# Kernel optimization log

Measured on AMD Instinct MI355X. Metric: run time of the kernel, lower is better.

The kernel has to match this reference:

```python
import jax, jax.numpy as jnp
import numpy as np

V, D, H, L, S_MAX = 32000, 1024, 16, 4, 1024
HD = D // H          # head dim = 64
FF = 4 * D           # mlp hidden = 4096
B, S = 2, 1024


def _layernorm(x, w, b, eps=1e-5):
    mu = jnp.mean(x, axis=-1, keepdims=True)
    var = jnp.mean(jnp.square(x - mu), axis=-1, keepdims=True)
    return (x - mu) * jax.lax.rsqrt(var + eps) * w + b


def setup_inputs() -> dict:
    key = jax.random.key(0)
    ks = jax.random.split(key, 16)
    r = lambda k, shape: (jax.random.normal(k, shape, dtype=jnp.float32) * 0.02)
    return {
        "input_ids": jax.random.randint(ks[0], (B, S), 0, V),
        "tok_emb": r(ks[1], (V, D)),
        "pos_emb": r(ks[2], (S_MAX, D)),
        "ln1_w": jnp.ones((L, D)), "ln1_b": jnp.zeros((L, D)),
        "ln2_w": jnp.ones((L, D)), "ln2_b": jnp.zeros((L, D)),
        "q_w": r(ks[3], (L, D, D)), "q_b": jnp.zeros((L, D)),
        "k_w": r(ks[4], (L, D, D)), "k_b": jnp.zeros((L, D)),
        "v_w": r(ks[5], (L, D, D)), "v_b": jnp.zeros((L, D)),
        "o_w": r(ks[6], (L, D, D)), "o_b": jnp.zeros((L, D)),
        "fc1_w": r(ks[7], (L, FF, D)), "fc1_b": jnp.zeros((L, FF)),
        "fc2_w": r(ks[8], (L, D, FF)), "fc2_b": jnp.zeros((L, D)),
        "lnf_w": jnp.ones((D,)), "lnf_b": jnp.zeros((D,)),
        "head_w": r(ks[9], (V, D)),
    }


def reference(input_ids, tok_emb, pos_emb, ln1_w, ln1_b, ln2_w, ln2_b,
              q_w, q_b, k_w, k_b, v_w, v_b, o_w, o_b,
              fc1_w, fc1_b, fc2_w, fc2_b, lnf_w, lnf_b, head_w):
    b, s = input_ids.shape
    x = tok_emb[input_ids] + pos_emb[:s][None, :, :]          # [B,S,D]
    causal = jnp.tril(jnp.ones((s, s), dtype=bool))           # [S,S]
    scale = 1.0 / np.sqrt(HD)
    for i in range(L):
        # --- causal MHA block ---
        h = _layernorm(x, ln1_w[i], ln1_b[i])
        q = (h @ q_w[i].T + q_b[i]).reshape(b, s, H, HD)
        k = (h @ k_w[i].T + k_b[i]).reshape(b, s, H, HD)
        v = (h @ v_w[i].T + v_b[i]).reshape(b, s, H, HD)
        scores = jnp.einsum('bqhd,bkhd->bhqk', q, k) * scale  # [B,H,S,S]
        scores = jnp.where(causal[None, None], scores, -jnp.inf)
        attn = jax.nn.softmax(scores, axis=-1)
        y = jnp.einsum('bhqk,bkhd->bqhd', attn, v).reshape(b, s, D)
        x = x + (y @ o_w[i].T + o_b[i])
        # --- GELU MLP block (exact gelu, matching torch F.gelu default) ---
        h = _layernorm(x, ln2_w[i], ln2_b[i])
        h = jax.nn.gelu(h @ fc1_w[i].T + fc1_b[i], approximate=False)
        x = x + (h @ fc2_w[i].T + fc2_b[i])
    x = _layernorm(x, lnf_w, lnf_b)
    logits = x[:, -1, :] @ head_w.T                           # [B,V]
    return logits
```

## Files before the change

### kernel.cpp

```cpp
#include <hip/hip_runtime.h>

#define V_SIZE 32000
#define D_DIM  1024
#define H_HEADS 16
#define L_LAYERS 4
#define HD_DIM 64
#define FF_DIM 4096
#define B_BATCH 2
#define S_SEQ  1024
#define M_ROWS (B_BATCH*S_SEQ)
#define KSPL   2

typedef short  s16x8 __attribute__((ext_vector_type(8)));
typedef unsigned short u16x8 __attribute__((ext_vector_type(8)));
typedef float  f32x4 __attribute__((ext_vector_type(4)));
typedef unsigned short u16;
typedef unsigned int   u32;

__device__ inline u16 f2bf(float f){
    u32 u = __float_as_uint(f);
    return (u16)((u + 0x7FFFu + ((u >> 16) & 1u)) >> 16);
}

__device__ inline float gelu_f(float v){
    float y = 0.7978845608f * (v + 0.044715f*v*v*v);
    y = fmaxf(-15.f, fminf(15.f, y));
    float u = __expf(-2.f*y);
    return v / (1.f + u);
}

__device__ inline char* lds_swz(void* base, int row, int byteoff){
    return (char*)base + row*128 + (byteoff ^ ((row & 7) << 4));
}

__device__ inline void gload16(const u16* g, u16* l){
    __builtin_amdgcn_global_load_lds(
        (const __attribute__((address_space(1))) void*)g,
        (__attribute__((address_space(3))) void*)l, 16, 0, 0);
}

__device__ inline int swz_src_col(int lin){
    int row = lin >> 3, s8 = lin & 7;
    return (s8*8) ^ ((row & 7) << 3);
}

__device__ inline s16x8 cvt8(float4 a, float4 b){
    s16x8 o;
    o[0]=(short)f2bf(a.x); o[1]=(short)f2bf(a.y);
    o[2]=(short)f2bf(a.z); o[3]=(short)f2bf(a.w);
    o[4]=(short)f2bf(b.x); o[5]=(short)f2bf(b.y);
    o[6]=(short)f2bf(b.z); o[7]=(short)f2bf(b.w);
    return o;
}

__global__ __launch_bounds__(256) void cvt_flat_k(
    const float* __restrict__ src, u16* __restrict__ dst)
{
    long i = ((long)blockIdx.x*256 + threadIdx.x) * 16;
    float4 v0 = *(const float4*)(src + i);
    float4 v1 = *(const float4*)(src + i + 4);
    float4 v2 = *(const float4*)(src + i + 8);
    float4 v3 = *(const float4*)(src + i + 12);
    *(s16x8*)(dst + i)     = cvt8(v0, v1);
    *(s16x8*)(dst + i + 8) = cvt8(v2, v3);
}

__global__ __launch_bounds__(256) void cvt_qkv_k(
    const float* __restrict__ qw, const float* __restrict__ kw,
    const float* __restrict__ vw, u16* __restrict__ dst)
{
    const long M1 = 1L << 20;
    const int which = blockIdx.y;
    const float* src = (which==0) ? qw : ((which==1) ? kw : vw);
    long i = ((long)blockIdx.x*256 + threadIdx.x) * 16;
    long layer = i >> 20, rem = i & (M1 - 1);
    u16* d = dst + layer*3*M1 + which*M1 + rem;
    float4 v0 = *(const float4*)(src + i);
    float4 v1 = *(const float4*)(src + i + 4);
    float4 v2 = *(const float4*)(src + i + 8);
    float4 v3 = *(const float4*)(src + i + 12);
    *(s16x8*)(d)     = cvt8(v0, v1);
    *(s16x8*)(d + 8) = cvt8(v2, v3);
}

__global__ __launch_bounds__(256) void embed_ln_k(
    const int* __restrict__ ids, const float* __restrict__ tok,
    const float* __restrict__ pos, const float* __restrict__ lw,
    const float* __restrict__ lb, float* __restrict__ x, u16* __restrict__ h)
{
    int row = blockIdx.x;
    int id  = ids[row];
    int s   = row & (S_SEQ - 1);
    int t   = threadIdx.x;
    float4 tv = *(const float4*)(tok + (size_t)id * D_DIM + t*4);
    float4 pv = *(const float4*)(pos + (size_t)s  * D_DIM + t*4);
    float4 vv;
    vv.x = tv.x + pv.x; vv.y = tv.y + pv.y; vv.z = tv.z + pv.z; vv.w = tv.w + pv.w;
    *(float4*)(x + (size_t)row * D_DIM + t*4) = vv;
    float sm  = vv.x + vv.y + vv.z + vv.w;
    float ss = vv.x*vv.x + vv.y*vv.y + vv.z*vv.z + vv.w*vv.w;
#pragma unroll
    for (int off = 1; off < 64; off <<= 1){
        sm += __shfl_xor(sm, off);
        ss += __shfl_xor(ss, off);
    }
    __shared__ float red[8];
    const int wid = t >> 6, lane = t & 63;
    if (lane == 0){ red[wid] = sm; red[4 + wid] = ss; }
    __syncthreads();
    sm = red[0] + red[1] + red[2] + red[3];
    ss = red[4] + red[5] + red[6] + red[7];
    float mu   = sm * (1.0f/1024.0f);
    float rstd = rsqrtf(ss * (1.0f/1024.0f) - mu*mu + 1e-5f);
    float4 wv = *(const float4*)(lw + t*4);
    float4 bv = *(const float4*)(lb + t*4);
    uint2 pk;
    pk.x = (u32)f2bf((vv.x-mu)*rstd*wv.x + bv.x) | ((u32)f2bf((vv.y-mu)*rstd*wv.y + bv.y) << 16);
    pk.y = (u32)f2bf((vv.z-mu)*rstd*wv.z + bv.z) | ((u32)f2bf((vv.w-mu)*rstd*wv.w + bv.w) << 16);
    *(uint2*)(h + (size_t)row * D_DIM + t*4) = pk;
}

__global__ __launch_bounds__(256) void layernorm_f_k(
    const float* __restrict__ x, const float* __restrict__ w, const float* __restrict__ bb,
    float* __restrict__ outF)
{
    const int row = blockIdx.x * S_SEQ + S_SEQ - 1;
    const int t = threadIdx.x;
    float4 vv = *(const float4*)(x + (size_t)row * D_DIM + t*4);
    float s  = vv.x + vv.y + vv.z + vv.w;
    float ss = vv.x*vv.x + vv.y*vv.y + vv.z*vv.z + vv.w*vv.w;
#pragma unroll
    for (int off = 1; off < 64; off <<= 1){
        s  += __shfl_xor(s,  off);
        ss += __shfl_xor(ss, off);
    }
    __shared__ float red[8];
    const int wid = t >> 6, lane = t & 63;
    if (lane == 0){ red[wid] = s; red[4 + wid] = ss; }
    __syncthreads();
    s  = red[0] + red[1] + red[2] + red[3];
    ss = red[4] + red[5] + red[6] + red[7];
    float mu   = s * (1.0f/1024.0f);
    float rstd = rsqrtf(ss * (1.0f/1024.0f) - mu*mu + 1e-5f);
    float4 wv = *(const float4*)(w  + t*4);
    float4 bv = *(const float4*)(bb + t*4);
    float4 o;
    o.x = (vv.x - mu)*rstd*wv.x + bv.x;
    o.y = (vv.y - mu)*rstd*wv.y + bv.y;
    o.z = (vv.z - mu)*rstd*wv.z + bv.z;
    o.w = (vv.w - mu)*rstd*wv.w + bv.w;
    *(float4*)(outF + (size_t)blockIdx.x * D_DIM + t*4) = o;
}

template<int DOLN>
__global__ __launch_bounds__(256) void reduce_ln_k(
    const float* __restrict__ part, const float* __restrict__ bias,
    float* __restrict__ x,
    const float* __restrict__ lw, const float* __restrict__ lb,
    u16* __restrict__ h)
{
    const int row = blockIdx.x, t = threadIdx.x;
    const size_t off = (size_t)row * D_DIM + t*4;
    float4 a = *(float4*)(x + off);
    float4 bv = *(const float4*)(bias + t*4);
    a.x += bv.x; a.y += bv.y; a.z += bv.z; a.w += bv.w;
#pragma unroll
    for (int si = 0; si < KSPL; si++){
        float4 pv = *(const float4*)(part + (size_t)si * M_ROWS * D_DIM + off);
        a.x += pv.x; a.y += pv.y; a.z += pv.z; a.w += pv.w;
    }
    *(float4*)(x + off) = a;
    if (DOLN){
        float sm = a.x + a.y + a.z + a.w;
        float ss = a.x*a.x + a.y*a.y + a.z*a.z + a.w*a.w;
#pragma unroll
        for (int o2 = 1; o2 < 64; o2 <<= 1){
            sm += __shfl_xor(sm, o2);
            ss += __shfl_xor(ss, o2);
        }
        __shared__ float red[8];
        const int wid = t >> 6, lane = t & 63;
        if (lane == 0){ red[wid] = sm; red[4 + wid] = ss; }
        __syncthreads();
        sm = red[0] + red[1] + red[2] + red[3];
        ss = red[4] + red[5] + red[6] + red[7];
        float mu   = sm * (1.0f/1024.0f);
        float rstd = rsqrtf(ss * (1.0f/1024.0f) - mu*mu + 1e-5f);
        float4 wv = *(const float4*)(lw + t*4);
        float4 lbv = *(const float4*)(lb + t*4);
        uint2 pk;
        pk.x = (u32)f2bf((a.x-mu)*rstd*wv.x + lbv.x) | ((u32)f2bf((a.y-mu)*rstd*wv.y + lbv.y) << 16);
        pk.y = (u32)f2bf((a.z-mu)*rstd*wv.z + lbv.z) | ((u32)f2bf((a.w-mu)*rstd*wv.w + lbv.w) << 16);
        *(uint2*)(h + (size_t)row * D_DIM + t*4) = pk;
    }
}

__global__ __launch_bounds__(256) void gemm_fc1_k(
    const u16* __restrict__ A, const u16* __restrict__ Bw,
    const float* __restrict__ b0, u16* __restrict__ outB, int Ndim, int Kdim)
{
    const int nx = gridDim.x, ny = gridDim.y;
    const int nwg = nx*ny;
    int orig = blockIdx.y*nx + blockIdx.x;
    int wg = (orig & 7)*(nwg >> 3) + (orig >> 3);
    const int bm = wg % nx;
    const int bn = wg / nx;

    const int nk = Kdim >> 6;

    __shared__ __align__(16) u16 As[2][128*64];
    __shared__ __align__(16) u16 Bs[2][128*64];

    const int t = threadIdx.x;
    const int wid = t >> 6, lane = t & 63, lr = lane & 15, lg = lane >> 4;
    const int wr = wid >> 1, wc = wid & 1;

    f32x4 acc[4][4];
#pragma unroll
    for (int m=0;m<4;m++)
#pragma unroll
        for (int n=0;n<4;n++) acc[m][n] = (f32x4){0.f,0.f,0.f,0.f};

    const u16* Abase = A  + (size_t)(bm*128)*Kdim;
    const u16* Bbase = Bw + (size_t)(bn*128)*Kdim;

    auto stage = [&](int koff, int buf){
#pragma unroll
        for (int i=0;i<4;i++){
            int lin = i*256 + t;
            int row = lin >> 3;
            int sc  = swz_src_col(lin);
            gload16(Abase + (size_t)row*Kdim + koff + sc, &As[buf][lin*8]);
        }
#pragma unroll
        for (int i=0;i<4;i++){
            int lin = i*256 + t;
            int row = lin >> 3;
            int sc  = swz_src_col(lin);
            gload16(Bbase + (size_t)row*Kdim + koff + sc, &Bs[buf][lin*8]);
        }
    };

    stage(0, 0);
    __syncthreads();
    int cb = 0;
    for (int ki = 0; ki < nk; ki++){
        if (ki+1 < nk) stage((ki+1)*64, cb^1);
#pragma unroll
        for (int kk=0;kk<2;kk++){
            s16x8 a[4], b[4];
#pragma unroll
            for (int m=0;m<4;m++)
                a[m] = *(s16x8*)lds_swz(As[cb], wr*64 + m*16 + lr, kk*64 + lg*16);
#pragma unroll
            for (int n=0;n<4;n++)
                b[n] = *(s16x8*)lds_swz(Bs[cb], wc*64 + n*16 + lr, kk*64 + lg*16);
#pragma unroll
            for (int m=0;m<4;m++)
#pragma unroll
                for (int n=0;n<4;n++)
                    acc[m][n] = __builtin_amdgcn_mfma_f32_16x16x32_bf16(a[m], b[n], acc[m][n], 0, 0, 0);
        }
        __syncthreads();
        cb ^= 1;
    }

#pragma unroll
    for (int n=0;n<4;n++){
        int col = bn*128 + wc*64 + n*16 + lr;
        float bvv = b0[col];
#pragma unroll
        for (int m=0;m<4;m++){
            int row0 = bm*128 + wr*64 + m*16 + lg*4;
#pragma unroll
            for (int j=0;j<4;j++){
                int row = row0 + j;
                float val = gelu_f(acc[m][n][j] + bvv);
                outB[(size_t)row * Ndim + col] = f2bf(val);
            }
        }
    }
}

__global__ __launch_bounds__(256) void gemm_qkv_k(
    const u16* __restrict__ A, const u16* __restrict__ Bw,
    const float* __restrict__ b0, const float* __restrict__ b1, const float* __restrict__ b2,
    u16* __restrict__ outB, int Ndim, int Kdim)
{
    const int nx = gridDim.x, ny = gridDim.y;
    const int nwg = nx*ny;
    int orig = blockIdx.y*nx + blockIdx.x;
    int wg = (orig & 7)*(nwg >> 3) + (orig >> 3);
    const int bm = wg % nx;
    const int bn = wg / nx;
    const int nk = Kdim >> 6;

    __shared__ __align__(16) u16 As[2][64*64];
    __shared__ __align__(16) u16 Bs[2][128*64];

    const int t = threadIdx.x;
    const int wid = t >> 6, lane = t & 63, lr = lane & 15, lg = lane >> 4;
    const int wr = wid >> 1, wc = wid & 1;

    f32x4 acc[2][4];
#pragma unroll
    for (int m=0;m<2;m++)
#pragma unroll
        for (int n=0;n<4;n++) acc[m][n] = (f32x4){0.f,0.f,0.f,0.f};

    const u16* Abase = A  + (size_t)(bm*64)*Kdim;
    const u16* Bbase = Bw + (size_t)(bn*128)*Kdim;

    auto stage = [&](int koff, int buf){
#pragma unroll
        for (int i=0;i<2;i++){
            int lin = i*256 + t;
            int row = lin >> 3;
            int sc  = swz_src_col(lin);
            gload16(Abase + (size_t)row*Kdim + koff + sc, &As[buf][lin*8]);
        }
#pragma unroll
        for (int i=0;i<4;i++){
            int lin = i*256 + t;
            int row = lin >> 3;
            int sc  = swz_src_col(lin);
            gload16(Bbase + (size_t)row*Kdim + koff + sc, &Bs[buf][lin*8]);
        }
    };

    stage(0, 0);
    __syncthreads();
    int cb = 0;
    for (int ki = 0; ki < nk; ki++){
        if (ki+1 < nk) stage((ki+1)*64, cb^1);
#pragma unroll
        for (int kk=0;kk<2;kk++){
            s16x8 a[2], b[4];
#pragma unroll
            for (int m=0;m<2;m++)
                a[m] = *(s16x8*)lds_swz(As[cb], wr*32 + m*16 + lr, kk*64 + lg*16);
#pragma unroll
            for (int n=0;n<4;n++)
                b[n] = *(s16x8*)lds_swz(Bs[cb], wc*64 + n*16 + lr, kk*64 + lg*16);
#pragma unroll
            for (int m=0;m<2;m++)
#pragma unroll
                for (int n=0;n<4;n++)
                    acc[m][n] = __builtin_amdgcn_mfma_f32_16x16x32_bf16(a[m], b[n], acc[m][n], 0, 0, 0);
        }
        __syncthreads();
        cb ^= 1;
    }

#pragma unroll
    for (int n=0;n<4;n++){
        int col = bn*128 + wc*64 + n*16 + lr;
        int which = col >> 10;
        const float* bp = (which==0) ? b0 : ((which==1) ? b1 : b2);
        float bvv = bp[col & 1023];
        float scl = (which == 0) ? 0.125f : 1.0f;
#pragma unroll
        for (int m=0;m<2;m++){
            int row0 = bm*64 + wr*32 + m*16 + lg*4;
#pragma unroll
            for (int j=0;j<4;j++){
                int row = row0 + j;
                float val = (acc[m][n][j] + bvv) * scl;
                outB[(size_t)row * Ndim + col] = f2bf(val);
            }
        }
    }
}

__global__ __launch_bounds__(256) void gemm64_k(
    const u16* __restrict__ A, const u16* __restrict__ Bw,
    float* __restrict__ outF, int Ndim, int Kdim, int kper)
{
    const int nx = gridDim.x, ny = gridDim.y;
    const int nwg = nx*ny*gridDim.z;
    int orig = (blockIdx.z*ny + blockIdx.y)*nx + blockIdx.x;
    int wg = (orig & 7)*(nwg >> 3) + (orig >> 3);
    const int bm = wg % nx; wg /= nx;
    const int bn = wg % ny;
    const int z  = wg / ny;
    const int kbeg = z * kper;
    const int nk = kper >> 6;

    __shared__ __align__(16) u16 As[2][64*64];
    __shared__ __align__(16) u16 Bs[2][128*64];

    const int t = threadIdx.x;
    const int wid = t >> 6, lane = t & 63, lr = lane & 15, lg = lane >> 4;
    const int wr = wid >> 1, wc = wid & 1;

    f32x4 acc[2][4];
#pragma unroll
    for (int m=0;m<2;m++)
#pragma unroll
        for (int n=0;n<4;n++) acc[m][n] = (f32x4){0.f,0.f,0.f,0.f};

    const u16* Abase = A  + (size_t)(bm*64)*Kdim + kbeg;
    const u16* Bbase = Bw + (size_t)(bn*128)*Kdim + kbeg;

    auto stage = [&](int koff, int buf){
#pragma unroll
        for (int i=0;i<2;i++){
            int lin = i*256 + t;
            int row = lin >> 3;
            int sc  = swz_src_col(lin);
            gload16(Abase + (size_t)row*Kdim + koff + sc, &As[buf][lin*8]);
        }
#pragma unroll
        for (int i=0;i<4;i++){
            int lin = i*256 + t;
            int row = lin >> 3;
            int sc  = swz_src_col(lin);
            gload16(Bbase + (size_t)row*Kdim + koff + sc, &Bs[buf][lin*8]);
        }
    };

    stage(0, 0);
    __syncthreads();
    int cb = 0;
    for (int ki = 0; ki < nk; ki++){
        if (ki+1 < nk) stage((ki+1)*64, cb^1);
#pragma unroll
        for (int kk=0;kk<2;kk++){
            s16x8 a[2], b[4];
#pragma unroll
            for (int m=0;m<2;m++)
                a[m] = *(s16x8*)lds_swz(As[cb], wr*32 + m*16 + lr, kk*64 + lg*16);
#pragma unroll
            for (int n=0;n<4;n++)
                b[n] = *(s16x8*)lds_swz(Bs[cb], wc*64 + n*16 + lr, kk*64 + lg*16);
#pragma unroll
            for (int m=0;m<2;m++)
#pragma unroll
                for (int n=0;n<4;n++)
                    acc[m][n] = __builtin_amdgcn_mfma_f32_16x16x32_bf16(a[m], b[n], acc[m][n], 0, 0, 0);
        }
        __syncthreads();
        cb ^= 1;
    }

#pragma unroll
    for (int n=0;n<4;n++){
        int col = bn*128 + wc*64 + n*16 + lr;
#pragma unroll
        for (int m=0;m<2;m++){
            int row0 = bm*64 + wr*32 + m*16 + lg*4;
#pragma unroll
            for (int j=0;j<4;j++){
                int row = row0 + j;
                outF[(size_t)z * M_ROWS * Ndim + (size_t)row * Ndim + col] = acc[m][n][j];
            }
        }
    }
}

__global__ __launch_bounds__(256) void attn_k(
    const u16* __restrict__ qkv, u16* __restrict__ y)
{
    const int gx = gridDim.x;
    const int nwg = gx * gridDim.y;
    int orig = blockIdx.y*gx + blockIdx.x;
    int wg = (orig & 7)*(nwg >> 3) + (orig >> 3);
    const int pairIdx = wg % gx;
    const int bh = wg / gx;
    const int b  = bh >> 4, h = bh & 15;

    __shared__ __align__(16) u16 Ks[2][64*64];
    __shared__ __align__(16) u16 VTs[2][64*64];
    __shared__ __align__(16) u16 Ps[4][16*64];

    const int t = threadIdx.x, wid = t >> 6, lane = t & 63, lr = lane & 15, lg = lane >> 4;
    const size_t rowb = (size_t)b * S_SEQ;
    const u16* qp = qkv + h*HD_DIM;
    const u16* kp = qkv + 1024 + h*HD_DIM;
    const u16* vp = qkv + 2048 + h*HD_DIM;

    const int kpr = t >> 3, dsl = t & 7;
    u16x8 vr0, vr1;

    auto issueK = [&](int kt, int buf){
#pragma unroll
        for (int i=0;i<2;i++){
            int lin = i*256 + t;
            int row = lin >> 3;
            int sc  = swz_src_col(lin);
            gload16(kp + (rowb + kt*64 + row)*3072 + sc, &Ks[buf][lin*8]);
        }
    };
    auto loadV = [&](int kt){
        vr0 = *(const u16x8*)(vp + (rowb + kt*64 + 2*kpr    )*3072 + dsl*8);
        vr1 = *(const u16x8*)(vp + (rowb + kt*64 + 2*kpr + 1)*3072 + dsl*8);
    };
    auto writeVT = [&](int buf){
#pragma unroll
        for (int j=0;j<8;j++){
            u32 pk = (u32)vr0[j] | ((u32)vr1[j] << 16);
            *(u32*)lds_swz(VTs[buf], dsl*8 + j, kpr*4) = pk;
        }
    };

#pragma unroll
    for (int ph = 0; ph < 2; ph++){
        const int s = ph ? (15 - pairIdx) : pairIdx;
        const int qw = s*64 + wid*16;
        s16x8 aq[2];
#pragma unroll
        for (int kc=0;kc<2;kc++)
            aq[kc] = *(const s16x8*)(qp + (rowb + qw + lr) * 3072 + kc*32 + lg*8);

        f32x4 o[4];
#pragma unroll
        for (int n=0;n<4;n++) o[n] = (f32x4){0.f,0.f,0.f,0.f};
        float lrun[4] = {0.f,0.f,0.f,0.f};

        const int nkv = s + 1;
        issueK(0, 0); loadV(0); writeVT(0);
        __syncthreads();
        int cb = 0;
        for (int kt = 0; kt < nkv; kt++){
            const bool more = (kt+1 < nkv);
            if (more){ issueK(kt+1, cb^1); loadV(kt+1); }

            f32x4 sf[4];
#pragma unroll
            for (int n=0;n<4;n++) sf[n] = (f32x4){0.f,0.f,0.f,0.f};
            __builtin_amdgcn_s_setprio(1);
#pragma unroll
            for (int kc=0;kc<2;kc++){
#pragma unroll
                for (int n=0;n<4;n++){
                    s16x8 bk = *(s16x8*)lds_swz(Ks[cb], n*16 + lr, kc*64 + lg*16);
                    sf[n] = __builtin_amdgcn_mfma_f32_16x16x32_bf16(aq[kc], bk, sf[n], 0, 0, 0);
                }
            }
            __builtin_amdgcn_s_setprio(0);
            const bool diag = (kt == s);
            float rs[4] = {0.f,0.f,0.f,0.f};
#pragma unroll
            for (int n=0;n<4;n++){
                int key = kt*64 + n*16 + lr;
#pragma unroll
                for (int j=0;j<4;j++){
                    float p = __expf(sf[n][j]);
                    if (diag && key > qw + lg*4 + j) p = 0.f;
                    sf[n][j] = p; rs[j] += p;
                }
            }
#pragma unroll
            for (int off=1; off<16; off<<=1){
#pragma unroll
                for (int j=0;j<4;j++) rs[j] += __shfl_xor(rs[j], off);
            }
#pragma unroll
            for (int j=0;j<4;j++) lrun[j] += rs[j];
            u16* Pw = Ps[wid];
#pragma unroll
            for (int n=0;n<4;n++)
#pragma unroll
                for (int j=0;j<4;j++)
                    *(u16*)lds_swz(Pw, lg*4 + j, (n*16 + lr)*2) = f2bf(sf[n][j]);
            __builtin_amdgcn_s_setprio(1);
#pragma unroll
            for (int kc=0;kc<2;kc++){
                s16x8 pa = *(s16x8*)lds_swz(Pw, lr, kc*64 + lg*16);
#pragma unroll
                for (int n=0;n<4;n++){
                    s16x8 bv = *(s16x8*)lds_swz(VTs[cb], n*16 + lr, kc*64 + lg*16);
                    o[n] = __builtin_amdgcn_mfma_f32_16x16x32_bf16(pa, bv, o[n], 0, 0, 0);
                }
            }
            __builtin_amdgcn_s_setprio(0);
            writeVT(cb^1);
            __syncthreads();
            cb ^= 1;
        }
        float inv[4];
#pragma unroll
        for (int j=0;j<4;j++) inv[j] = 1.0f / lrun[j];
#pragma unroll
        for (int n=0;n<4;n++)
#pragma unroll
            for (int j=0;j<4;j++)
                y[(rowb + qw + lg*4 + j) * D_DIM + h*HD_DIM + n*16 + lr] = f2bf(o[n][j] * inv[j]);
        __syncthreads();
    }
}

__global__ __launch_bounds__(256) void head_k(
    const float* __restrict__ xf, const float* __restrict__ hw, float* __restrict__ out)
{
    __shared__ float xs[2*D_DIM];
    int t = threadIdx.x;
#pragma unroll
    for (int i=0;i<2;i++){
        int j = t + i*256;
        *(float4*)&xs[j*4] = *(const float4*)(xf + j*4);
    }
    __syncthreads();
    int wid = t >> 6, lane = t & 63;
    int vrow = blockIdx.x * 4 + wid;
    float s0 = 0.f, s1 = 0.f;
#pragma unroll
    for (int it=0; it<4; it++){
        int j = it*64 + lane;
        float4 w4 = *(const float4*)(hw + (size_t)vrow * D_DIM + j*4);
        float4 x0 = *(const float4*)&xs[j*4];
        float4 x1 = *(const float4*)&xs[D_DIM + j*4];
        s0 += w4.x*x0.x + w4.y*x0.y + w4.z*x0.z + w4.w*x0.w;
        s1 += w4.x*x1.x + w4.y*x1.y + w4.z*x1.z + w4.w*x1.w;
    }
#pragma unroll
    for (int off=1; off<64; off<<=1){
        s0 += __shfl_xor(s0, off);
        s1 += __shfl_xor(s1, off);
    }
    if (lane == 0){
        out[vrow]          = s0;
        out[V_SIZE + vrow] = s1;
    }
}

extern "C" void kernel_launch(void* const* d_in, const int* in_sizes, int n_in,
                              void* d_out, int out_size, void* d_ws, size_t ws_size,
                              hipStream_t stream)
{
    (void)in_sizes; (void)n_in; (void)out_size; (void)ws_size;
    const int*   ids  = (const int*)  d_in[0];
    const float* tok  = (const float*)d_in[1];
    const float* pos  = (const float*)d_in[2];
    const float* ln1w = (const float*)d_in[3];
    const float* ln1b = (const float*)d_in[4];
    const float* ln2w = (const float*)d_in[5];
    const float* ln2b = (const float*)d_in[6];
    const float* qw   = (const float*)d_in[7];
    const float* qbi  = (const float*)d_in[8];
    const float* kw   = (const float*)d_in[9];
    const float* kbi  = (const float*)d_in[10];
    const float* vw   = (const float*)d_in[11];
    const float* vbi  = (const float*)d_in[12];
    const float* ow   = (const float*)d_in[13];
    const float* obi  = (const float*)d_in[14];
    const float* f1w  = (const float*)d_in[15];
    const float* f1b  = (const float*)d_in[16];
    const float* f2w  = (const float*)d_in[17];
    const float* f2b  = (const float*)d_in[18];
    const float* lnfw = (const float*)d_in[19];
    const float* lnfb = (const float*)d_in[20];
    const float* hw   = (const float*)d_in[21];

    const long MD = (long)1024*1024;
    char* p = (char*)d_ws;
    float* x    = (float*)p; p += (size_t)M_ROWS * D_DIM * 4;
    u16* h      = (u16*)p;   p += (size_t)M_ROWS * D_DIM * 2;
    u16* qkvbuf = (u16*)p;   p += (size_t)M_ROWS * 3072 * 2;
    u16* ybuf   = (u16*)p;   p += (size_t)M_ROWS * D_DIM * 2;
    u16* h1     = (u16*)p;   p += (size_t)M_ROWS * FF_DIM * 2;
    float* part = (float*)p; p += (size_t)KSPL * M_ROWS * D_DIM * 4;
    u16* wbuf   = (u16*)p;   p += (size_t)48 * MD * 2;
    float* xf   = (float*)p; p += (size_t)2 * D_DIM * 4;
    float* logits = (float*)d_out;

    u16* w_qkv = wbuf;
    u16* w_o   = wbuf + 12*MD;
    u16* w_f1  = wbuf + 16*MD;
    u16* w_f2  = wbuf + 32*MD;

    cvt_qkv_k <<<dim3(1024, 3), 256, 0, stream>>>(qw, kw, vw, w_qkv);
    cvt_flat_k<<<dim3(1024),    256, 0, stream>>>(ow,  w_o);
    cvt_flat_k<<<dim3(4096),    256, 0, stream>>>(f1w, w_f1);
    cvt_flat_k<<<dim3(4096),    256, 0, stream>>>(f2w, w_f2);

    embed_ln_k<<<dim3(M_ROWS), 256, 0, stream>>>(ids, tok, pos, ln1w, ln1b, x, h);

    for (int i = 0; i < L_LAYERS; i++){
        gemm_qkv_k<<<dim3(32, 24), 256, 0, stream>>>(
            h, w_qkv + (size_t)i*3*MD,
            qbi + i*D_DIM, kbi + i*D_DIM, vbi + i*D_DIM,
            qkvbuf, 3072, D_DIM);
        attn_k<<<dim3(8, 32), 256, 0, stream>>>(qkvbuf, ybuf);
        gemm64_k<<<dim3(32, 8, KSPL), 256, 0, stream>>>(
            ybuf, w_o + (size_t)i*MD, part, D_DIM, D_DIM, D_DIM/KSPL);
        reduce_ln_k<1><<<dim3(M_ROWS), 256, 0, stream>>>(
            part, obi + i*D_DIM, x, ln2w + i*D_DIM, ln2b + i*D_DIM, h);
        gemm_fc1_k<<<dim3(16, 32), 256, 0, stream>>>(
            h, w_f1 + (size_t)i*4*MD, f1b + i*FF_DIM, h1, FF_DIM, D_DIM);
        gemm64_k<<<dim3(32, 8, KSPL), 256, 0, stream>>>(
            h1, w_f2 + (size_t)i*4*MD, part, D_DIM, FF_DIM, FF_DIM/KSPL);
        if (i < L_LAYERS-1){
            reduce_ln_k<1><<<dim3(M_ROWS), 256, 0, stream>>>(
                part, f2b + i*D_DIM, x, ln1w + (i+1)*D_DIM, ln1b + (i+1)*D_DIM, h);
        } else {
            reduce_ln_k<0><<<dim3(M_ROWS), 256, 0, stream>>>(
                part, f2b + i*D_DIM, x, nullptr, nullptr, nullptr);
        }
    }

    layernorm_f_k<<<dim3(B_BATCH), 256, 0, stream>>>(x, lnfw, lnfb, xf);
    head_k<<<dim3(V_SIZE/4), 256, 0, stream>>>(xf, hw, logits);
}
```

Baseline: 646.3 us.

## Replace split-K output GEMMs with 64x64 tiles fusing bias and residual add

The o-proj and fc2 GEMMs drop split-K over two partial buffers. They now use 64x64 output tiles (512 blocks instead of 256x2) and add the bias and residual directly into x in the epilogue. The separate reduce kernel becomes a plain layernorm kernel, and the last layer skips it entirely. This removes the fp32 partial-buffer write and read traffic, at the cost of smaller tiles with less operand reuse and a longer K loop per block.

```diff
diff --git a/kernel.cpp b/kernel.cpp
--- a/kernel.cpp
+++ b/kernel.cpp
@@ -9,7 +9,6 @@
 #define B_BATCH 2
 #define S_SEQ  1024
 #define M_ROWS (B_BATCH*S_SEQ)
-#define KSPL   2
 
 typedef short  s16x8 __attribute__((ext_vector_type(8)));
 typedef unsigned short u16x8 __attribute__((ext_vector_type(8)));
@@ -117,6 +116,35 @@
     uint2 pk;
     pk.x = (u32)f2bf((vv.x-mu)*rstd*wv.x + bv.x) | ((u32)f2bf((vv.y-mu)*rstd*wv.y + bv.y) << 16);
     pk.y = (u32)f2bf((vv.z-mu)*rstd*wv.z + bv.z) | ((u32)f2bf((vv.w-mu)*rstd*wv.w + bv.w) << 16);
+    *(uint2*)(h + (size_t)row * D_DIM + t*4) = pk;
+}
+
+__global__ __launch_bounds__(256) void ln_k(
+    const float* __restrict__ x, const float* __restrict__ lw,
+    const float* __restrict__ lb, u16* __restrict__ h)
+{
+    const int row = blockIdx.x, t = threadIdx.x;
+    float4 a = *(const float4*)(x + (size_t)row * D_DIM + t*4);
+    float sm = a.x + a.y + a.z + a.w;
+    float ss = a.x*a.x + a.y*a.y + a.z*a.z + a.w*a.w;
+#pragma unroll
+    for (int o2 = 1; o2 < 64; o2 <<= 1){
+        sm += __shfl_xor(sm, o2);
+        ss += __shfl_xor(ss, o2);
+    }
+    __shared__ float red[8];
+    const int wid = t >> 6, lane = t & 63;
+    if (lane == 0){ red[wid] = sm; red[4 + wid] = ss; }
+    __syncthreads();
+    sm = red[0] + red[1] + red[2] + red[3];
+    ss = red[4] + red[5] + red[6] + red[7];
+    float mu   = sm * (1.0f/1024.0f);
+    float rstd = rsqrtf(ss * (1.0f/1024.0f) - mu*mu + 1e-5f);
+    float4 wv  = *(const float4*)(lw + t*4);
+    float4 lbv = *(const float4*)(lb + t*4);
+    uint2 pk;
+    pk.x = (u32)f2bf((a.x-mu)*rstd*wv.x + lbv.x) | ((u32)f2bf((a.y-mu)*rstd*wv.y + lbv.y) << 16);
+    pk.y = (u32)f2bf((a.z-mu)*rstd*wv.z + lbv.z) | ((u32)f2bf((a.w-mu)*rstd*wv.w + lbv.w) << 16);
     *(uint2*)(h + (size_t)row * D_DIM + t*4) = pk;
 }
 
@@ -152,49 +180,6 @@
     *(float4*)(outF + (size_t)blockIdx.x * D_DIM + t*4) = o;
 }
 
-template<int DOLN>
-__global__ __launch_bounds__(256) void reduce_ln_k(
-    const float* __restrict__ part, const float* __restrict__ bias,
-    float* __restrict__ x,
-    const float* __restrict__ lw, const float* __restrict__ lb,
-    u16* __restrict__ h)
-{
-    const int row = blockIdx.x, t = threadIdx.x;
-    const size_t off = (size_t)row * D_DIM + t*4;
-    float4 a = *(float4*)(x + off);
-    float4 bv = *(const float4*)(bias + t*4);
-    a.x += bv.x; a.y += bv.y; a.z += bv.z; a.w += bv.w;
-#pragma unroll
-    for (int si = 0; si < KSPL; si++){
-        float4 pv = *(const float4*)(part + (size_t)si * M_ROWS * D_DIM + off);
-        a.x += pv.x; a.y += pv.y; a.z += pv.z; a.w += pv.w;
-    }
-    *(float4*)(x + off) = a;
-    if (DOLN){
-        float sm = a.x + a.y + a.z + a.w;
-        float ss = a.x*a.x + a.y*a.y + a.z*a.z + a.w*a.w;
-#pragma unroll
-        for (int o2 = 1; o2 < 64; o2 <<= 1){
-            sm += __shfl_xor(sm, o2);
-            ss += __shfl_xor(ss, o2);
-        }
-        __shared__ float red[8];
-        const int wid = t >> 6, lane = t & 63;
-        if (lane == 0){ red[wid] = sm; red[4 + wid] = ss; }
-        __syncthreads();
-        sm = red[0] + red[1] + red[2] + red[3];
-        ss = red[4] + red[5] + red[6] + red[7];
-        float mu   = sm * (1.0f/1024.0f);
-        float rstd = rsqrtf(ss * (1.0f/1024.0f) - mu*mu + 1e-5f);
-        float4 wv = *(const float4*)(lw + t*4);
-        float4 lbv = *(const float4*)(lb + t*4);
-        uint2 pk;
-        pk.x = (u32)f2bf((a.x-mu)*rstd*wv.x + lbv.x) | ((u32)f2bf((a.y-mu)*rstd*wv.y + lbv.y) << 16);
-        pk.y = (u32)f2bf((a.z-mu)*rstd*wv.z + lbv.z) | ((u32)f2bf((a.w-mu)*rstd*wv.w + lbv.w) << 16);
-        *(uint2*)(h + (size_t)row * D_DIM + t*4) = pk;
-    }
-}
-
 __global__ __launch_bounds__(256) void gemm_fc1_k(
     const u16* __restrict__ A, const u16* __restrict__ Bw,
     const float* __restrict__ b0, u16* __restrict__ outB, int Ndim, int Kdim)
@@ -372,35 +357,33 @@
     }
 }
 
-__global__ __launch_bounds__(256) void gemm64_k(
+__global__ __launch_bounds__(256) void gemm_res_k(
     const u16* __restrict__ A, const u16* __restrict__ Bw,
-    float* __restrict__ outF, int Ndim, int Kdim, int kper)
+    const float* __restrict__ bias, float* __restrict__ x, int Kdim)
 {
     const int nx = gridDim.x, ny = gridDim.y;
-    const int nwg = nx*ny*gridDim.z;
-    int orig = (blockIdx.z*ny + blockIdx.y)*nx + blockIdx.x;
+    const int nwg = nx*ny;
+    int orig = blockIdx.y*nx + blockIdx.x;
     int wg = (orig & 7)*(nwg >> 3) + (orig >> 3);
-    const int bm = wg % nx; wg /= nx;
-    const int bn = wg % ny;
-    const int z  = wg / ny;
-    const int kbeg = z * kper;
-    const int nk = kper >> 6;
+    const int bm = wg % nx;
+    const int bn = wg / nx;
+    const int nk = Kdim >> 6;
 
     __shared__ __align__(16) u16 As[2][64*64];
-    __shared__ __align__(16) u16 Bs[2][128*64];
+    __shared__ __align__(16) u16 Bs[2][64*64];
 
     const int t = threadIdx.x;
     const int wid = t >> 6, lane = t & 63, lr = lane & 15, lg = lane >> 4;
     const int wr = wid >> 1, wc = wid & 1;
 
-    f32x4 acc[2][4];
+    f32x4 acc[2][2];
 #pragma unroll
     for (int m=0;m<2;m++)
 #pragma unroll
-        for (int n=0;n<4;n++) acc[m][n] = (f32x4){0.f,0.f,0.f,0.f};
-
-    const u16* Abase = A  + (size_t)(bm*64)*Kdim + kbeg;
-    const u16* Bbase = Bw + (size_t)(bn*128)*Kdim + kbeg;
+        for (int n=0;n<2;n++) acc[m][n] = (f32x4){0.f,0.f,0.f,0.f};
+
+    const u16* Abase = A  + (size_t)(bm*64)*Kdim;
+    const u16* Bbase = Bw + (size_t)(bn*64)*Kdim;
 
     auto stage = [&](int koff, int buf){
 #pragma unroll
@@ -411,7 +394,7 @@
             gload16(Abase + (size_t)row*Kdim + koff + sc, &As[buf][lin*8]);
         }
 #pragma unroll
-        for (int i=0;i<4;i++){
+        for (int i=0;i<2;i++){
             int lin = i*256 + t;
             int row = lin >> 3;
             int sc  = swz_src_col(lin);
@@ -426,17 +409,17 @@
         if (ki+1 < nk) stage((ki+1)*64, cb^1);
 #pragma unroll
         for (int kk=0;kk<2;kk++){
-            s16x8 a[2], b[4];
+            s16x8 a[2], b[2];
 #pragma unroll
             for (int m=0;m<2;m++)
                 a[m] = *(s16x8*)lds_swz(As[cb], wr*32 + m*16 + lr, kk*64 + lg*16);
 #pragma unroll
-            for (int n=0;n<4;n++)
-                b[n] = *(s16x8*)lds_swz(Bs[cb], wc*64 + n*16 + lr, kk*64 + lg*16);
+            for (int n=0;n<2;n++)
+                b[n] = *(s16x8*)lds_swz(Bs[cb], wc*32 + n*16 + lr, kk*64 + lg*16);
 #pragma unroll
             for (int m=0;m<2;m++)
 #pragma unroll
-                for (int n=0;n<4;n++)
+                for (int n=0;n<2;n++)
                     acc[m][n] = __builtin_amdgcn_mfma_f32_16x16x32_bf16(a[m], b[n], acc[m][n], 0, 0, 0);
         }
         __syncthreads();
@@ -444,15 +427,16 @@
     }
 
 #pragma unroll
-    for (int n=0;n<4;n++){
-        int col = bn*128 + wc*64 + n*16 + lr;
+    for (int n=0;n<2;n++){
+        int col = bn*64 + wc*32 + n*16 + lr;
+        float bvv = bias[col];
 #pragma unroll
         for (int m=0;m<2;m++){
             int row0 = bm*64 + wr*32 + m*16 + lg*4;
 #pragma unroll
             for (int j=0;j<4;j++){
-                int row = row0 + j;
-                outF[(size_t)z * M_ROWS * Ndim + (size_t)row * Ndim + col] = acc[m][n][j];
+                size_t idx = (size_t)(row0 + j) * D_DIM + col;
+                x[idx] += acc[m][n][j] + bvv;
             }
         }
     }
@@ -659,7 +643,6 @@
     u16* qkvbuf = (u16*)p;   p += (size_t)M_ROWS * 3072 * 2;
     u16* ybuf   = (u16*)p;   p += (size_t)M_ROWS * D_DIM * 2;
     u16* h1     = (u16*)p;   p += (size_t)M_ROWS * FF_DIM * 2;
-    float* part = (float*)p; p += (size_t)KSPL * M_ROWS * D_DIM * 4;
     u16* wbuf   = (u16*)p;   p += (size_t)48 * MD * 2;
     float* xf   = (float*)p; p += (size_t)2 * D_DIM * 4;
     float* logits = (float*)d_out;
@@ -682,20 +665,17 @@
             qbi + i*D_DIM, kbi + i*D_DIM, vbi + i*D_DIM,
             qkvbuf, 3072, D_DIM);
         attn_k<<<dim3(8, 32), 256, 0, stream>>>(qkvbuf, ybuf);
-        gemm64_k<<<dim3(32, 8, KSPL), 256, 0, stream>>>(
-            ybuf, w_o + (size_t)i*MD, part, D_DIM, D_DIM, D_DIM/KSPL);
-        reduce_ln_k<1><<<dim3(M_ROWS), 256, 0, stream>>>(
-            part, obi + i*D_DIM, x, ln2w + i*D_DIM, ln2b + i*D_DIM, h);
+        gemm_res_k<<<dim3(32, 16), 256, 0, stream>>>(
+            ybuf, w_o + (size_t)i*MD, obi + i*D_DIM, x, D_DIM);
+        ln_k<<<dim3(M_ROWS), 256, 0, stream>>>(
+            x, ln2w + i*D_DIM, ln2b + i*D_DIM, h);
         gemm_fc1_k<<<dim3(16, 32), 256, 0, stream>>>(
             h, w_f1 + (size_t)i*4*MD, f1b + i*FF_DIM, h1, FF_DIM, D_DIM);
-        gemm64_k<<<dim3(32, 8, KSPL), 256, 0, stream>>>(
-            h1, w_f2 + (size_t)i*4*MD, part, D_DIM, FF_DIM, FF_DIM/KSPL);
+        gemm_res_k<<<dim3(32, 16), 256, 0, stream>>>(
+            h1, w_f2 + (size_t)i*4*MD, f2b + i*D_DIM, x, FF_DIM);
         if (i < L_LAYERS-1){
-            reduce_ln_k<1><<<dim3(M_ROWS), 256, 0, stream>>>(
-                part, f2b + i*D_DIM, x, ln1w + (i+1)*D_DIM, ln1b + (i+1)*D_DIM, h);
-        } else {
-            reduce_ln_k<0><<<dim3(M_ROWS), 256, 0, stream>>>(
-                part, f2b + i*D_DIM, x, nullptr, nullptr, nullptr);
+            ln_k<<<dim3(M_ROWS), 256, 0, stream>>>(
+                x, ln1w + (i+1)*D_DIM, ln1b + (i+1)*D_DIM, h);
         }
     }
 
```

After: 684.6 us. +5.9%, slower.

## Share K/V tiles between paired query strips in attention and fuse weight conversions

Applied to the files above, without the earlier changes.

The attention kernel previously handled its two causal-balanced query strips one after another, loading K/V tiles separately for each. It now runs both strips in a single pass over the KV tiles, so each loaded tile serves the high strip and, while still in range, the low strip. This halves K/V loads and barrier rounds, at the cost of more live registers for two sets of accumulators and Q fragments. Separately, the four weight-conversion launches are merged into one kernel to cut launch overhead.

```diff
diff --git a/kernel.cpp b/kernel.cpp
--- a/kernel.cpp
+++ b/kernel.cpp
@@ -53,32 +53,33 @@
     return o;
 }
 
-__global__ __launch_bounds__(256) void cvt_flat_k(
-    const float* __restrict__ src, u16* __restrict__ dst)
-{
-    long i = ((long)blockIdx.x*256 + threadIdx.x) * 16;
-    float4 v0 = *(const float4*)(src + i);
-    float4 v1 = *(const float4*)(src + i + 4);
-    float4 v2 = *(const float4*)(src + i + 8);
-    float4 v3 = *(const float4*)(src + i + 12);
-    *(s16x8*)(dst + i)     = cvt8(v0, v1);
-    *(s16x8*)(dst + i + 8) = cvt8(v2, v3);
-}
-
-__global__ __launch_bounds__(256) void cvt_qkv_k(
+__global__ __launch_bounds__(256) void cvt_all_k(
     const float* __restrict__ qw, const float* __restrict__ kw,
-    const float* __restrict__ vw, u16* __restrict__ dst)
+    const float* __restrict__ vw, const float* __restrict__ ow,
+    const float* __restrict__ f1w, const float* __restrict__ f2w,
+    u16* __restrict__ w_qkv, u16* __restrict__ w_o,
+    u16* __restrict__ w_f1, u16* __restrict__ w_f2)
 {
     const long M1 = 1L << 20;
-    const int which = blockIdx.y;
-    const float* src = (which==0) ? qw : ((which==1) ? kw : vw);
-    long i = ((long)blockIdx.x*256 + threadIdx.x) * 16;
-    long layer = i >> 20, rem = i & (M1 - 1);
-    u16* d = dst + layer*3*M1 + which*M1 + rem;
-    float4 v0 = *(const float4*)(src + i);
-    float4 v1 = *(const float4*)(src + i + 4);
-    float4 v2 = *(const float4*)(src + i + 8);
-    float4 v3 = *(const float4*)(src + i + 12);
+    const int bx = blockIdx.x;
+    const float* s; u16* d; long i;
+    if (bx < 3072){
+        int which = bx >> 10;
+        s = (which==0) ? qw : ((which==1) ? kw : vw);
+        i = ((long)(bx & 1023)*256 + threadIdx.x) * 16;
+        long layer = i >> 20, rem = i & (M1 - 1);
+        d = w_qkv + layer*3*M1 + which*M1 + rem;
+    } else if (bx < 4096){
+        s = ow;  i = ((long)(bx-3072)*256 + threadIdx.x) * 16; d = w_o  + i;
+    } else if (bx < 8192){
+        s = f1w; i = ((long)(bx-4096)*256 + threadIdx.x) * 16; d = w_f1 + i;
+    } else {
+        s = f2w; i = ((long)(bx-8192)*256 + threadIdx.x) * 16; d = w_f2 + i;
+    }
+    float4 v0 = *(const float4*)(s + i);
+    float4 v1 = *(const float4*)(s + i + 4);
+    float4 v2 = *(const float4*)(s + i + 8);
+    float4 v3 = *(const float4*)(s + i + 12);
     *(s16x8*)(d)     = cvt8(v0, v1);
     *(s16x8*)(d + 8) = cvt8(v2, v3);
 }
@@ -465,9 +466,12 @@
     const int nwg = gx * gridDim.y;
     int orig = blockIdx.y*gx + blockIdx.x;
     int wg = (orig & 7)*(nwg >> 3) + (orig >> 3);
-    const int pairIdx = wg % gx;
+    const int p  = wg % gx;
     const int bh = wg / gx;
     const int b  = bh >> 4, h = bh & 15;
+
+    const int s_lo = p, s_hi = 15 - p;
+    const int ntiles = s_hi + 1;
 
     __shared__ __align__(16) u16 Ks[2][64*64];
     __shared__ __align__(16) u16 VTs[2][64*64];
@@ -478,6 +482,21 @@
     const u16* qp = qkv + h*HD_DIM;
     const u16* kp = qkv + 1024 + h*HD_DIM;
     const u16* vp = qkv + 2048 + h*HD_DIM;
+
+    const int qw_lo = s_lo*64 + wid*16;
+    const int qw_hi = s_hi*64 + wid*16;
+
+    s16x8 aq_lo[2], aq_hi[2];
+#pragma unroll
+    for (int kc=0;kc<2;kc++){
+        aq_lo[kc] = *(const s16x8*)(qp + (rowb + qw_lo + lr) * 3072 + kc*32 + lg*8);
+        aq_hi[kc] = *(const s16x8*)(qp + (rowb + qw_hi + lr) * 3072 + kc*32 + lg*8);
+    }
+
+    f32x4 o_lo[4], o_hi[4];
+#pragma unroll
+    for (int n=0;n<4;n++){ o_lo[n] = (f32x4){0.f,0.f,0.f,0.f}; o_hi[n] = (f32x4){0.f,0.f,0.f,0.f}; }
+    float l_lo[4] = {0.f,0.f,0.f,0.f}, l_hi[4] = {0.f,0.f,0.f,0.f};
 
     const int kpr = t >> 3, dsl = t & 7;
     u16x8 vr0, vr1;
@@ -503,91 +522,83 @@
         }
     };
 
-#pragma unroll
-    for (int ph = 0; ph < 2; ph++){
-        const int s = ph ? (15 - pairIdx) : pairIdx;
-        const int qw = s*64 + wid*16;
-        s16x8 aq[2];
-#pragma unroll
-        for (int kc=0;kc<2;kc++)
-            aq[kc] = *(const s16x8*)(qp + (rowb + qw + lr) * 3072 + kc*32 + lg*8);
-
-        f32x4 o[4];
-#pragma unroll
-        for (int n=0;n<4;n++) o[n] = (f32x4){0.f,0.f,0.f,0.f};
-        float lrun[4] = {0.f,0.f,0.f,0.f};
-
-        const int nkv = s + 1;
-        issueK(0, 0); loadV(0); writeVT(0);
+    auto doStrip = [&](const s16x8* aq, f32x4* o, float* lsum, int qwS, int kt, bool diag, int cb){
+        f32x4 sf[4];
+#pragma unroll
+        for (int n=0;n<4;n++) sf[n] = (f32x4){0.f,0.f,0.f,0.f};
+        __builtin_amdgcn_s_setprio(1);
+#pragma unroll
+        for (int kc=0;kc<2;kc++){
+#pragma unroll
+            for (int n=0;n<4;n++){
+                s16x8 bk = *(s16x8*)lds_swz(Ks[cb], n*16 + lr, kc*64 + lg*16);
+                sf[n] = __builtin_amdgcn_mfma_f32_16x16x32_bf16(aq[kc], bk, sf[n], 0, 0, 0);
+            }
+        }
+        __builtin_amdgcn_s_setprio(0);
+        float rs[4] = {0.f,0.f,0.f,0.f};
+#pragma unroll
+        for (int n=0;n<4;n++){
+            int key = kt*64 + n*16 + lr;
+#pragma unroll
+            for (int j=0;j<4;j++){
+                float pe = __expf(sf[n][j]);
+                if (diag && key > qwS + lg*4 + j) pe = 0.f;
+                sf[n][j] = pe; rs[j] += pe;
+            }
+        }
+#pragma unroll
+        for (int off=1; off<16; off<<=1){
+#pragma unroll
+            for (int j=0;j<4;j++) rs[j] += __shfl_xor(rs[j], off);
+        }
+#pragma unroll
+        for (int j=0;j<4;j++) lsum[j] += rs[j];
+        u16* Pw = Ps[wid];
+#pragma unroll
+        for (int n=0;n<4;n++)
+#pragma unroll
+            for (int j=0;j<4;j++)
+                *(u16*)lds_swz(Pw, lg*4 + j, (n*16 + lr)*2) = f2bf(sf[n][j]);
+        __builtin_amdgcn_s_setprio(1);
+#pragma unroll
+        for (int kc=0;kc<2;kc++){
+            s16x8 pa = *(s16x8*)lds_swz(Pw, lr, kc*64 + lg*16);
+#pragma unroll
+            for (int n=0;n<4;n++){
+                s16x8 bv = *(s16x8*)lds_swz(VTs[cb], n*16 + lr, kc*64 + lg*16);
+                o[n] = __builtin_amdgcn_mfma_f32_16x16x32_bf16(pa, bv, o[n], 0, 0, 0);
+            }
+        }
+        __builtin_amdgcn_s_setprio(0);
+    };
+
+    issueK(0, 0); loadV(0); writeVT(0);
+    __syncthreads();
+    int cb = 0;
+    for (int kt = 0; kt < ntiles; kt++){
+        const bool more = (kt+1 < ntiles);
+        if (more){ issueK(kt+1, cb^1); loadV(kt+1); }
+
+        doStrip(aq_hi, o_hi, l_hi, qw_hi, kt, kt == s_hi, cb);
+        if (kt <= s_lo)
+            doStrip(aq_lo, o_lo, l_lo, qw_lo, kt, kt == s_lo, cb);
+
+        if (more) writeVT(cb^1);
         __syncthreads();
-        int cb = 0;
-        for (int kt = 0; kt < nkv; kt++){
-            const bool more = (kt+1 < nkv);
-            if (more){ issueK(kt+1, cb^1); loadV(kt+1); }
-
-            f32x4 sf[4];
-#pragma unroll
-            for (int n=0;n<4;n++) sf[n] = (f32x4){0.f,0.f,0.f,0.f};
-            __builtin_amdgcn_s_setprio(1);
-#pragma unroll
-            for (int kc=0;kc<2;kc++){
-#pragma unroll
-                for (int n=0;n<4;n++){
-                    s16x8 bk = *(s16x8*)lds_swz(Ks[cb], n*16 + lr, kc*64 + lg*16);
-                    sf[n] = __builtin_amdgcn_mfma_f32_16x16x32_bf16(aq[kc], bk, sf[n], 0, 0, 0);
-                }
-            }
-            __builtin_amdgcn_s_setprio(0);
-            const bool diag = (kt == s);
-            float rs[4] = {0.f,0.f,0.f,0.f};
-#pragma unroll
-            for (int n=0;n<4;n++){
-                int key = kt*64 + n*16 + lr;
-#pragma unroll
-                for (int j=0;j<4;j++){
-                    float p = __expf(sf[n][j]);
-                    if (diag && key > qw + lg*4 + j) p = 0.f;
-                    sf[n][j] = p; rs[j] += p;
-                }
-            }
-#pragma unroll
-            for (int off=1; off<16; off<<=1){
-#pragma unroll
-                for (int j=0;j<4;j++) rs[j] += __shfl_xor(rs[j], off);
-            }
-#pragma unroll
-            for (int j=0;j<4;j++) lrun[j] += rs[j];
-            u16* Pw = Ps[wid];
-#pragma unroll
-            for (int n=0;n<4;n++)
-#pragma unroll
-                for (int j=0;j<4;j++)
-                    *(u16*)lds_swz(Pw, lg*4 + j, (n*16 + lr)*2) = f2bf(sf[n][j]);
-            __builtin_amdgcn_s_setprio(1);
-#pragma unroll
-            for (int kc=0;kc<2;kc++){
-                s16x8 pa = *(s16x8*)lds_swz(Pw, lr, kc*64 + lg*16);
-#pragma unroll
-                for (int n=0;n<4;n++){
-                    s16x8 bv = *(s16x8*)lds_swz(VTs[cb], n*16 + lr, kc*64 + lg*16);
-                    o[n] = __builtin_amdgcn_mfma_f32_16x16x32_bf16(pa, bv, o[n], 0, 0, 0);
-                }
-            }
-            __builtin_amdgcn_s_setprio(0);
-            writeVT(cb^1);
-            __syncthreads();
-            cb ^= 1;
-        }
-        float inv[4];
-#pragma unroll
-        for (int j=0;j<4;j++) inv[j] = 1.0f / lrun[j];
-#pragma unroll
-        for (int n=0;n<4;n++)
-#pragma unroll
-            for (int j=0;j<4;j++)
-                y[(rowb + qw + lg*4 + j) * D_DIM + h*HD_DIM + n*16 + lr] = f2bf(o[n][j] * inv[j]);
-        __syncthreads();
-    }
+        cb ^= 1;
+    }
+
+    float inv_lo[4], inv_hi[4];
+#pragma unroll
+    for (int j=0;j<4;j++){ inv_lo[j] = 1.0f / l_lo[j]; inv_hi[j] = 1.0f / l_hi[j]; }
+#pragma unroll
+    for (int n=0;n<4;n++)
+#pragma unroll
+        for (int j=0;j<4;j++){
+            y[(rowb + qw_hi + lg*4 + j) * D_DIM + h*HD_DIM + n*16 + lr] = f2bf(o_hi[n][j] * inv_hi[j]);
+            y[(rowb + qw_lo + lg*4 + j) * D_DIM + h*HD_DIM + n*16 + lr] = f2bf(o_lo[n][j] * inv_lo[j]);
+        }
 }
 
 __global__ __launch_bounds__(256) void head_k(
@@ -669,10 +680,8 @@
     u16* w_f1  = wbuf + 16*MD;
     u16* w_f2  = wbuf + 32*MD;
 
-    cvt_qkv_k <<<dim3(1024, 3), 256, 0, stream>>>(qw, kw, vw, w_qkv);
-    cvt_flat_k<<<dim3(1024),    256, 0, stream>>>(ow,  w_o);
-    cvt_flat_k<<<dim3(4096),    256, 0, stream>>>(f1w, w_f1);
-    cvt_flat_k<<<dim3(4096),    256, 0, stream>>>(f2w, w_f2);
+    cvt_all_k<<<dim3(12288), 256, 0, stream>>>(
+        qw, kw, vw, ow, f1w, f2w, w_qkv, w_o, w_f1, w_f2);
 
     embed_ln_k<<<dim3(M_ROWS), 256, 0, stream>>>(ids, tok, pos, ln1w, ln1b, x, h);
 
```

Result: faster. 631.3 us (-2.3%).
